# Kernel optimization log

Hardware: AMD Instinct MI355X
Metric: run time of the kernel (lower is better)

The kernel has to match this reference:

```python
import jax, jax.numpy as jnp
import numpy as np

R = 25          # regions (hard-coded [:25, 0] slice in the source)
NUM_CONSUMER = 27


def _ln(x, g, b, axes, eps):
    m = jnp.mean(x, axis=axes, keepdims=True)
    v = jnp.mean((x - m) ** 2, axis=axes, keepdims=True)
    return (x - m) / jnp.sqrt(v + eps) * g + b


def setup_inputs() -> dict:
    key = jax.random.key(0)
    n, c, h, e = 64, 64, 8, 1024
    bs = R
    ks = jax.random.split(key, 24)
    inp = {
        "business_structure_target": jax.random.normal(ks[0], (bs, c, n, 4), jnp.float32),
        "business_structure_infected": jax.random.normal(ks[1], (bs, c, n, 4), jnp.float32),
        "customer_structure_target": jax.random.uniform(ks[2], (bs, c, n, NUM_CONSUMER, 4), jnp.float32),
        "customer_structure_infected": jax.random.uniform(ks[3], (bs, c, n, NUM_CONSUMER, 4), jnp.float32),
        "index_target_idx": jax.random.randint(ks[4], (bs, c), 0, R, jnp.int32),
        "index_infected_idx": jax.random.randint(ks[5], (bs, c), 0, R, jnp.int32),
        "covid_outbreak_business": jax.random.randint(ks[6], (bs, c), 0, n, jnp.int32),
        # parameters
        "emb_weight": jax.random.normal(ks[7], (R * n, e), jnp.float32),
        "emb_ln_g": jnp.ones((e,), jnp.float32),
        "emb_ln_b": jnp.zeros((e,), jnp.float32),
        "WQ_t": jax.random.normal(ks[8], (h, e, e), jnp.float32) / np.sqrt(e),
        "WK_t": jax.random.normal(ks[9], (h, e, e), jnp.float32) / np.sqrt(e),
        "WQ_i": jax.random.normal(ks[10], (h, e, e), jnp.float32) / np.sqrt(e),
        "WK_i": jax.random.normal(ks[11], (h, e, e), jnp.float32) / np.sqrt(e),
        "W_os": jax.random.normal(ks[12], (e, e), jnp.float32) / np.sqrt(e),
        "b_os": jnp.zeros((e,), jnp.float32),
        "BS_g": jnp.ones((c, n), jnp.float32), "BS_b": jnp.zeros((c, n), jnp.float32),
        "CS_g": jnp.ones((c, n), jnp.float32), "CS_b": jnp.zeros((c, n), jnp.float32),
        "OS_g": jnp.ones((c, n), jnp.float32), "OS_b": jnp.zeros((c, n), jnp.float32),
    }
    return inp


def _mha(emb_blocks, WQ, WK, indices):
    # emb_blocks: (R, n, e); indices: (d,)
    d = indices.shape[0]
    n, e = emb_blocks.shape[1], emb_blocks.shape[2]
    ew = emb_blocks[indices].reshape(d * n, e)           # gather district blocks
    Q = jnp.einsum('te,hfe->htf', ew, WQ).reshape(-1, d, n, e)  # torch Linear: x @ W.T
    K = jnp.einsum('te,hfe->htf', ew, WK).reshape(-1, d, n, e)
    QK = jnp.einsum('hdie,hdje->hdij', Q, K) / jnp.sqrt(jnp.float32(e))
    # torch Softmax(dim=1) on (d, n, n) -> normalize over the first industry axis
    return jax.nn.softmax(QK, axis=2)                    # (h, d, n, n)


def reference(business_structure_target, business_structure_infected,
              customer_structure_target, customer_structure_infected,
              index_target_idx, index_infected_idx, covid_outbreak_business,
              emb_weight, emb_ln_g, emb_ln_b,
              WQ_t, WK_t, WQ_i, WK_i, W_os, b_os,
              BS_g, BS_b, CS_g, CS_b, OS_g, OS_b):
    n = business_structure_target.shape[2]
    e = emb_weight.shape[1]

    bt = jnp.mean(business_structure_target, -1)[:R, 0]      # (R, n)
    bi = jnp.mean(business_structure_infected, -1)[0]        # (c, n)
    ct = jnp.mean(customer_structure_target, -1)[:R, 0]      # (R, n, 27)
    ci = jnp.mean(customer_structure_infected, -1)[0]        # (c, n, 27)

    emb_norm = _ln(emb_weight, emb_ln_g, emb_ln_b, -1, 1e-16)
    emb_blocks = emb_norm.reshape(R, n, e)

    idx_t = index_target_idx[:R, 0].astype(jnp.int32)        # (R,)
    idx_i = index_infected_idx[0].astype(jnp.int32)          # (c,)

    attn_t = _mha(emb_blocks, WQ_t, WK_t, idx_t)             # (h, R, n, n)
    BR_trg = jnp.einsum('di,hdij->djh', bt, attn_t)          # (R, n, h)
    attn_i = _mha(emb_blocks, WQ_i, WK_i, idx_i)             # (h, c, n, n)
    BR_inf = jnp.einsum('di,hdij->djh', bi, attn_i)          # (c, n, h)

    # cosine similarity over the head dim, broadcast (R,1,n,h) x (1,c,n,h)
    eps = 1e-15
    a = BR_trg[:, None]
    b = BR_inf[None]
    dot = jnp.sum(a * b, -1)
    na = jnp.maximum(jnp.sqrt(jnp.sum(a * a, -1)), eps)
    nb = jnp.maximum(jnp.sqrt(jnp.sum(b * b, -1)), eps)
    BS = dot / (na * nb)                                     # (R, c, n)

    # JSD-style customer-structure similarity
    lt = jax.nn.log_softmax(ct, -1)[:, None]                 # (R, 1, n, 27)
    li = jax.nn.log_softmax(ci, -1)[None]                    # (1, c, n, 27)
    M = jax.nn.log_softmax((lt + li) / 2, -1)
    expM = jnp.exp(M)
    # KLDivLoss(log_target=True): exp(target) * (target - input)
    kl_t = jnp.mean(expM * (M - lt), -1)
    kl_i = jnp.mean(expM * (M - li), -1)
    CS = -((kl_t + kl_i) / 2)                                # (R, c, n)

    # outbreak-business similarity
    cov_buz = covid_outbreak_business[0].astype(jnp.int32)   # (c,)
    inf_emb_idx = idx_i * n + cov_buz
    ob_emb = emb_weight[inf_emb_idx] @ W_os.T + b_os         # (c, e)
    OS = (ob_emb @ emb_weight.T).reshape(-1, R, n)           # (c, R, n)
    OS = jnp.transpose(OS, (1, 0, 2))                        # (R, c, n)

    BS = _ln(BS, BS_g, BS_b, (-2, -1), 1e-5)
    CS = _ln(CS, CS_g, CS_b, (-2, -1), 1e-5)
    OS = _ln(OS, OS_g, OS_b, (-2, -1), 1e-5)
    return (BS, CS, OS)
```

## Files before the change

### kernel.cpp

```cpp
#include <hip/hip_runtime.h>
#include <math.h>

#define RR 25
#define HH 8
#define EE 1024
#define NCN 27

typedef short bf16x8 __attribute__((ext_vector_type(8)));
typedef float f32x4 __attribute__((ext_vector_type(4)));
typedef unsigned short us4 __attribute__((ext_vector_type(4)));
typedef unsigned short us8 __attribute__((ext_vector_type(8)));

__device__ __forceinline__ unsigned short f2bf(float x) {
    union { float f; unsigned int u; } v; v.f = x;
    const unsigned int u = v.u;
    return (unsigned short)((u + 0x7fffu + ((u >> 16) & 1u)) >> 16);
}
__device__ __forceinline__ float bf2f(unsigned short h) {
    union { unsigned int u; float f; } v; v.u = ((unsigned int)h) << 16;
    return v.f;
}

__device__ __forceinline__ float block_reduce_sum_256(float v, float* red) {
#pragma unroll
    for (int off = 32; off > 0; off >>= 1) v += __shfl_down(v, off, 64);
    const int lane = threadIdx.x & 63, wid = threadIdx.x >> 6;
    if (lane == 0) red[wid] = v;
    __syncthreads();
    if (threadIdx.x == 0) red[0] = red[0] + red[1] + red[2] + red[3];
    __syncthreads();
    const float r = red[0];
    __syncthreads();
    return r;
}

#define WTEN 16777216ull
#define WHEAD 2097152ull

__global__ __launch_bounds__(256) void k_ln_emb(
    const float* __restrict__ emb, const float* __restrict__ g,
    const float* __restrict__ b, float* __restrict__ out,
    unsigned short* __restrict__ Apl)
{
    __shared__ float red[4];
    const int t = blockIdx.x;
    const float* row = emb + (size_t)t * EE;
    float4 x = reinterpret_cast<const float4*>(row)[threadIdx.x];
    float s = x.x + x.y + x.z + x.w;
    s = block_reduce_sum_256(s, red);
    const float m = s * (1.0f / 1024.0f);
    const float d0 = x.x - m, d1 = x.y - m, d2 = x.z - m, d3 = x.w - m;
    float sq = d0*d0 + d1*d1 + d2*d2 + d3*d3;
    sq = block_reduce_sum_256(sq, red);
    const float rs = rsqrtf(sq * (1.0f / 1024.0f) + 1e-16f);
    const float4 gv = reinterpret_cast<const float4*>(g)[threadIdx.x];
    const float4 bv = reinterpret_cast<const float4*>(b)[threadIdx.x];
    float o[4];
    o[0] = d0 * rs * gv.x + bv.x;
    o[1] = d1 * rs * gv.y + bv.y;
    o[2] = d2 * rs * gv.z + bv.z;
    o[3] = d3 * rs * gv.w + bv.w;
    float4 of; of.x = o[0]; of.y = o[1]; of.z = o[2]; of.w = o[3];
    reinterpret_cast<float4*>(out + (size_t)t * EE)[threadIdx.x] = of;
    us4 hv, lv;
#pragma unroll
    for (int j = 0; j < 4; ++j) {
        const unsigned short h = f2bf(o[j]);
        hv[j] = h; lv[j] = f2bf(o[j] - bf2f(h));
    }
    const int k0 = threadIdx.x * 4;
    const int kt = k0 >> 5, kc = (k0 >> 3) & 3, j0 = k0 & 7;
    const int lane = (t & 15) + 16 * kc;
    const size_t base = ((size_t)(kt * 100 + (t >> 4)) * 2) * 512 + lane * 8 + j0;
    *reinterpret_cast<us4*>(Apl + base)       = hv;
    *reinterpret_cast<us4*>(Apl + base + 512) = lv;
}

__global__ __launch_bounds__(256) void k_splitw(
    const float* __restrict__ w0, const float* __restrict__ w1,
    const float* __restrict__ w2, const float* __restrict__ w3,
    unsigned short* __restrict__ wsp)
{
    const int t = blockIdx.y;
    const float* src = (t == 0) ? w0 : ((t == 1) ? w1 : ((t == 2) ? w2 : w3));
    unsigned short* dst = wsp + (size_t)t * WTEN;
    const size_t q = (size_t)blockIdx.x * 256 + threadIdx.x;
    const float4 x = reinterpret_cast<const float4*>(src)[q];
    const float xf[4] = {x.x, x.y, x.z, x.w};
    us4 hv, lv;
#pragma unroll
    for (int j = 0; j < 4; ++j) {
        const unsigned short h = f2bf(xf[j]);
        hv[j] = h; lv[j] = f2bf(xf[j] - bf2f(h));
    }
    const size_t e4 = q * 4;
    const int h = (int)(e4 >> 20);
    const int rem = (int)(e4 & 1048575);
    const int f = rem >> 10, e = rem & 1023;
    const int kt = e >> 5, kc = (e >> 3) & 3, j0 = e & 7;
    const int lane = (f & 15) + 16 * kc;
    const size_t base = (size_t)h * WHEAD + ((size_t)(kt * 64 + (f >> 4)) * 2) * 512 + lane * 8 + j0;
    *reinterpret_cast<us4*>(dst + base)       = hv;
    *reinterpret_cast<us4*>(dst + base + 512) = lv;
}

__global__ __launch_bounds__(256) void k_proj2(
    const unsigned short* __restrict__ Apl,
    const unsigned short* __restrict__ Wpl,
    float* __restrict__ Qb, float* __restrict__ Kb)
{
    __shared__ __align__(16) unsigned short As_l[8 * 512];
    __shared__ __align__(16) unsigned short Bs_l[32 * 512];
    const int fid = blockIdx.x;
    const int xcd = fid & 7;
    const int iw = fid >> 3;
    const int z = xcd + (iw / 100) * 8;
    const int mb = iw % 100;
    const int by = mb >> 2, bx = mb & 3;
    const int pk = z >> 3, h = z & 7;
    const unsigned short* Wb = Wpl + (size_t)pk * WTEN + (size_t)h * WHEAD;
    float* C = (pk ? Kb : Qb) + (size_t)h * 1600 * EE;
    const int tid = threadIdx.x;
    const int lane = tid & 63, wv = tid >> 6;
    const int by4 = by * 4, bx16 = bx * 16;
    f32x4 acc[4][4] = {};
    for (int kt = 0; kt < 32; ++kt) {
        const unsigned short* aslab = Apl + ((size_t)(kt * 100 + by4)) * 1024;
        const unsigned short* bslab = Wb  + ((size_t)(kt * 64  + bx16)) * 1024;
        us8 ra0 = *reinterpret_cast<const us8*>(aslab + (size_t)tid * 8);
        us8 ra1 = *reinterpret_cast<const us8*>(aslab + (size_t)(256 + tid) * 8);
        us8 rb[8];
#pragma unroll
        for (int c = 0; c < 8; ++c)
            rb[c] = *reinterpret_cast<const us8*>(bslab + (size_t)(c * 256 + tid) * 8);
        __syncthreads();
        *reinterpret_cast<us8*>(As_l + tid * 8) = ra0;
        *reinterpret_cast<us8*>(As_l + (256 + tid) * 8) = ra1;
#pragma unroll
        for (int c = 0; c < 8; ++c)
            *reinterpret_cast<us8*>(Bs_l + (c * 256 + tid) * 8) = rb[c];
        __syncthreads();
        bf16x8 ah[4], al[4], bh[4], bl[4];
#pragma unroll
        for (int m = 0; m < 4; ++m) {
            ah[m] = *reinterpret_cast<const bf16x8*>(As_l + (m * 2 + 0) * 512 + lane * 8);
            al[m] = *reinterpret_cast<const bf16x8*>(As_l + (m * 2 + 1) * 512 + lane * 8);
        }
#pragma unroll
        for (int n = 0; n < 4; ++n) {
            const int nt = wv * 4 + n;
            bh[n] = *reinterpret_cast<const bf16x8*>(Bs_l + (nt * 2 + 0) * 512 + lane * 8);
            bl[n] = *reinterpret_cast<const bf16x8*>(Bs_l + (nt * 2 + 1) * 512 + lane * 8);
        }
#pragma unroll
        for (int m = 0; m < 4; ++m)
#pragma unroll
            for (int n = 0; n < 4; ++n) {
                acc[m][n] = __builtin_amdgcn_mfma_f32_16x16x32_bf16(ah[m], bh[n], acc[m][n], 0, 0, 0);
                acc[m][n] = __builtin_amdgcn_mfma_f32_16x16x32_bf16(ah[m], bl[n], acc[m][n], 0, 0, 0);
                acc[m][n] = __builtin_amdgcn_mfma_f32_16x16x32_bf16(al[m], bh[n], acc[m][n], 0, 0, 0);
            }
    }
    const int rg = lane >> 4, fr = lane & 15;
#pragma unroll
    for (int m = 0; m < 4; ++m)
#pragma unroll
        for (int n = 0; n < 4; ++n)
#pragma unroll
            for (int q = 0; q < 4; ++q) {
                const int row = by * 64 + m * 16 + rg * 4 + q;
                const int col = bx * 256 + wv * 64 + n * 16 + fr;
                C[(size_t)row * EE + col] = acc[m][n][q];
            }
}

struct SplitTiles {
    unsigned short Ah[64][40], Al[64][40], Bh[64][40], Bl[64][40];
};

#define MFMA_COMPUTE(SM)                                                         \
    {                                                                            \
        bf16x8 ah_[2], al_[2], bh_[2], bl_[2];                                   \
        _Pragma("unroll")                                                        \
        for (int m = 0; m < 2; ++m) {                                            \
            const int r = wr * 32 + m * 16 + fr;                                 \
            ah_[m] = *reinterpret_cast<const bf16x8*>(&(SM).Ah[r][ch * 8]);      \
            al_[m] = *reinterpret_cast<const bf16x8*>(&(SM).Al[r][ch * 8]);      \
        }                                                                        \
        _Pragma("unroll")                                                        \
        for (int n = 0; n < 2; ++n) {                                            \
            const int r = wc * 32 + n * 16 + fr;                                 \
            bh_[n] = *reinterpret_cast<const bf16x8*>(&(SM).Bh[r][ch * 8]);      \
            bl_[n] = *reinterpret_cast<const bf16x8*>(&(SM).Bl[r][ch * 8]);      \
        }                                                                        \
        _Pragma("unroll")                                                        \
        for (int m = 0; m < 2; ++m)                                              \
            _Pragma("unroll")                                                    \
            for (int n = 0; n < 2; ++n) {                                        \
                acc[m][n] = __builtin_amdgcn_mfma_f32_16x16x32_bf16(ah_[m], bh_[n], acc[m][n], 0, 0, 0); \
                acc[m][n] = __builtin_amdgcn_mfma_f32_16x16x32_bf16(ah_[m], bl_[n], acc[m][n], 0, 0, 0); \
                acc[m][n] = __builtin_amdgcn_mfma_f32_16x16x32_bf16(al_[m], bh_[n], acc[m][n], 0, 0, 0); \
            }                                                                    \
    }

#define MFMA_STAGE_SPLIT_GEN(AROW, BROW, SM)                                     \
    {                                                                            \
        float4 ra[2], rb[2];                                                     \
        _Pragma("unroll")                                                        \
        for (int l = 0; l < 2; ++l) {                                            \
            const int id = l * 256 + tid;                                        \
            const int row = id >> 3, c4 = (id & 7) * 4;                          \
            ra[l] = *reinterpret_cast<const float4*>((AROW(row)) + k0 + c4);     \
            rb[l] = *reinterpret_cast<const float4*>((BROW(row)) + k0 + c4);     \
        }                                                                        \
        __syncthreads();                                                         \
        _Pragma("unroll")                                                        \
        for (int l = 0; l < 2; ++l) {                                            \
            const int id = l * 256 + tid;                                        \
            const int row = id >> 3, c4 = (id & 7) * 4;                          \
            const float xa[4] = {ra[l].x, ra[l].y, ra[l].z, ra[l].w};            \
            const float xb[4] = {rb[l].x, rb[l].y, rb[l].z, rb[l].w};            \
            us4 ahv, alv, bhv, blv;                                              \
            _Pragma("unroll")                                                    \
            for (int j = 0; j < 4; ++j) {                                        \
                const unsigned short ha = f2bf(xa[j]);                           \
                ahv[j] = ha; alv[j] = f2bf(xa[j] - bf2f(ha));                    \
                const unsigned short hb = f2bf(xb[j]);                           \
                bhv[j] = hb; blv[j] = f2bf(xb[j] - bf2f(hb));                    \
            }                                                                    \
            *reinterpret_cast<us4*>(&(SM).Ah[row][c4]) = ahv;                    \
            *reinterpret_cast<us4*>(&(SM).Al[row][c4]) = alv;                    \
            *reinterpret_cast<us4*>(&(SM).Bh[row][c4]) = bhv;                    \
            *reinterpret_cast<us4*>(&(SM).Bl[row][c4]) = blv;                    \
        }                                                                        \
        __syncthreads();                                                         \
    }

__global__ __launch_bounds__(256) void k_proj_mfma(
    const float* __restrict__ A,
    const float* __restrict__ WQ, const float* __restrict__ WK,
    float* __restrict__ Qb, float* __restrict__ Kb, int qkHeadStride)
{
    __shared__ __align__(16) SplitTiles sm;
    const int h = blockIdx.z >> 1;
    const int pk = blockIdx.z & 1;
    const float* W = (pk ? WK : WQ) + (size_t)h * EE * EE;
    float* C = (pk ? Kb : Qb) + (size_t)h * qkHeadStride;
    const int bx = blockIdx.x, by = blockIdx.y;
    const int tid = threadIdx.x;
    const int lane = tid & 63, w = tid >> 6;
    const int wr = w >> 1, wc = w & 1;
    const int fr = lane & 15, ch = lane >> 4;
    const float* Abase = A + (size_t)by * 64 * EE;
    const float* Bbase = W + (size_t)bx * 64 * EE;
#define AROWP(r) (Abase + (size_t)(r) * EE)
#define BROWP(r) (Bbase + (size_t)(r) * EE)
    f32x4 acc[2][2] = {};
    for (int k0 = 0; k0 < EE; k0 += 32) {
        MFMA_STAGE_SPLIT_GEN(AROWP, BROWP, sm)
        MFMA_COMPUTE(sm)
    }
#undef AROWP
#undef BROWP
    const int rg = lane >> 4;
#pragma unroll
    for (int m = 0; m < 2; ++m)
#pragma unroll
        for (int n = 0; n < 2; ++n)
#pragma unroll
            for (int q = 0; q < 4; ++q) {
                const int row = by * 64 + wr * 32 + m * 16 + rg * 4 + q;
                const int col = bx * 64 + wc * 32 + n * 16 + fr;
                C[(size_t)row * EE + col] = acc[m][n][q];
            }
}

__global__ __launch_bounds__(256) void k_qk_mfma(
    const float* __restrict__ Qall, const float* __restrict__ Kall,
    float* __restrict__ attn_all, int qkHeadStride, int attnHeadStride)
{
    __shared__ __align__(16) union { SplitTiles t; float Ss[64][65]; } u;
    __shared__ float redm[4][64];
    __shared__ float reds[4][64];
    const int r = blockIdx.x;
    const int h = blockIdx.y;
    const float* Q = Qall + (size_t)h * qkHeadStride;
    const float* K = Kall + (size_t)h * qkHeadStride;
    float* attn = attn_all + (size_t)h * attnHeadStride + (size_t)r * 4096;
    const int tid = threadIdx.x;
    const int lane = tid & 63, w = tid >> 6;
    const int wr = w >> 1, wc = w & 1;
    const int fr = lane & 15, ch = lane >> 4;
    const float* Abase = Q + (size_t)r * 64 * EE;
    const float* Bbase = K + (size_t)r * 64 * EE;
#define AROWP(rr) (Abase + (size_t)(rr) * EE)
#define BROWP(rr) (Bbase + (size_t)(rr) * EE)
    f32x4 acc[2][2] = {};
    for (int k0 = 0; k0 < EE; k0 += 32) {
        MFMA_STAGE_SPLIT_GEN(AROWP, BROWP, u.t)
        MFMA_COMPUTE(u.t)
    }
#undef AROWP
#undef BROWP
    __syncthreads();
    const int rg = lane >> 4;
#pragma unroll
    for (int m = 0; m < 2; ++m)
#pragma unroll
        for (int n = 0; n < 2; ++n)
#pragma unroll
            for (int q = 0; q < 4; ++q)
                u.Ss[wr * 32 + m * 16 + rg * 4 + q][wc * 32 + n * 16 + fr] =
                    acc[m][n][q] * (1.0f / 32.0f);
    __syncthreads();
    const int j = tid & 63, seg = tid >> 6;
    float mx = -1e30f;
#pragma unroll
    for (int i = 0; i < 16; ++i) mx = fmaxf(mx, u.Ss[seg * 16 + i][j]);
    redm[seg][j] = mx;
    __syncthreads();
    const float cm = fmaxf(fmaxf(redm[0][j], redm[1][j]), fmaxf(redm[2][j], redm[3][j]));
    float ssum = 0.f;
#pragma unroll
    for (int i = 0; i < 16; ++i) {
        const float e = __expf(u.Ss[seg * 16 + i][j] - cm);
        u.Ss[seg * 16 + i][j] = e;
        ssum += e;
    }
    reds[seg][j] = ssum;
    __syncthreads();
    const float inv = 1.0f / (reds[0][j] + reds[1][j] + reds[2][j] + reds[3][j]);
#pragma unroll
    for (int i = 0; i < 16; ++i)
        attn[(seg * 16 + i) * 64 + j] = u.Ss[seg * 16 + i][j] * inv;
}

__global__ __launch_bounds__(64) void k_br(
    const float* __restrict__ bst, const float* __restrict__ bsi,
    const int* __restrict__ iti, const int* __restrict__ iii,
    const float* __restrict__ attn_t, const float* __restrict__ attn_i,
    float* __restrict__ br_t, float* __restrict__ br_i)
{
    __shared__ float bw[64];
    const int dp = blockIdx.x;
    const int h = blockIdx.y;
    const int j = threadIdx.x;
    const float* attn;
    float* out;
    if (dp < RR) {
        const int d = dp;
        const int rb = iti[d * 64];
        const float* p = bst + ((size_t)(d * 64) * 64 + j) * 4;
        bw[j] = 0.25f * (p[0] + p[1] + p[2] + p[3]);
        attn = attn_t + ((size_t)h * RR + rb) * 4096;
        out = br_t + (size_t)d * 64 * 8;
    } else {
        const int d = dp - RR;
        const int rb = iii[d];
        const float* p = bsi + ((size_t)d * 64 + j) * 4;
        bw[j] = 0.25f * (p[0] + p[1] + p[2] + p[3]);
        attn = attn_i + ((size_t)h * RR + rb) * 4096;
        out = br_i + (size_t)d * 64 * 8;
    }
    __syncthreads();
    float acc = 0.f;
#pragma unroll 8
    for (int i = 0; i < 64; ++i) acc += bw[i] * attn[i * 64 + j];
    out[(size_t)j * 8 + h] = acc;
}

__global__ __launch_bounds__(256) void k_bs(
    const float* __restrict__ br_t, const float* __restrict__ br_i,
    float* __restrict__ raw)
{
    const int p = blockIdx.x;
#pragma unroll
    for (int it = 0; it < 16; ++it) {
        const int o = it * 256 + threadIdx.x;
        const int q = o >> 6, j = o & 63;
        const float* a = br_t + ((size_t)p * 64 + j) * 8;
        const float* b = br_i + ((size_t)q * 64 + j) * 8;
        float dot = 0.f, sa = 0.f, sb = 0.f;
#pragma unroll
        for (int h = 0; h < 8; ++h) {
            const float va = a[h], vb = b[h];
            dot += va * vb; sa += va * va; sb += vb * vb;
        }
        const float na = fmaxf(sqrtf(sa), 1e-15f);
        const float nb = fmaxf(sqrtf(sb), 1e-15f);
        raw[(size_t)p * 4096 + o] = dot / (na * nb);
    }
}

__global__ __launch_bounds__(256) void k_lsm(
    const float* __restrict__ cst, const float* __restrict__ csi,
    float* __restrict__ lt, float* __restrict__ li)
{
    const int row = blockIdx.x * 256 + threadIdx.x;
    if (row >= 1600 + 4096) return;
    const float* src;
    float* dst;
    if (row < 1600) {
        const int d = row >> 6, i = row & 63;
        src = cst + ((size_t)(d * 64) * 64 + i) * NCN * 4;
        dst = lt + (size_t)row * NCN;
    } else {
        const int u = row - 1600;
        const int q = u >> 6, i = u & 63;
        src = csi + ((size_t)q * 64 + i) * NCN * 4;
        dst = li + (size_t)u * NCN;
    }
    float x[NCN];
    float m = -1e30f;
#pragma unroll
    for (int k = 0; k < NCN; ++k) {
        x[k] = 0.25f * (src[k*4] + src[k*4+1] + src[k*4+2] + src[k*4+3]);
        m = fmaxf(m, x[k]);
    }
    float s = 0.f;
#pragma unroll
    for (int k = 0; k < NCN; ++k) s += __expf(x[k] - m);
    const float lse = m + __logf(s);
#pragma unroll
    for (int k = 0; k < NCN; ++k) dst[k] = x[k] - lse;
}

__global__ __launch_bounds__(256) void k_cs(
    const float* __restrict__ lt, const float* __restrict__ li, float* __restrict__ raw)
{
    const int p = blockIdx.x;
    for (int it = 0; it < 16; ++it) {
        const int o = it * 256 + threadIdx.x;
        const int q = o >> 6, i = o & 63;
        const float* a = lt + ((size_t)p * 64 + i) * NCN;
        const float* b = li + ((size_t)q * 64 + i) * NCN;
        float la[NCN], lb[NCN];
        float m = -1e30f;
#pragma unroll
        for (int k = 0; k < NCN; ++k) {
            la[k] = a[k]; lb[k] = b[k];
            m = fmaxf(m, 0.5f * (la[k] + lb[k]));
        }
        float z = 0.f;
#pragma unroll
        for (int k = 0; k < NCN; ++k) z += __expf(0.5f * (la[k] + lb[k]) - m);
        const float lse = m + __logf(z);
        float kt = 0.f, ki = 0.f;
#pragma unroll
        for (int k = 0; k < NCN; ++k) {
            const float M = 0.5f * (la[k] + lb[k]) - lse;
            const float eM = __expf(M);
            kt += eM * (M - la[k]);
            ki += eM * (M - lb[k]);
        }
        raw[(size_t)p * 4096 + o] = -(kt + ki) * (0.5f / 27.0f);
    }
}

__global__ __launch_bounds__(256) void k_obemb2(
    const float* __restrict__ emb, const float* __restrict__ Wos,
    const float* __restrict__ bos, const int* __restrict__ iii,
    const int* __restrict__ cob, float* __restrict__ ob)
{
    __shared__ __align__(16) SplitTiles sm;
    __shared__ int gidx[64];
    const int bx = blockIdx.x;
    const int tid = threadIdx.x;
    const int lane = tid & 63, w = tid >> 6;
    const int wr = w >> 1, wc = w & 1;
    const int fr = lane & 15, ch = lane >> 4;
    if (tid < 64) gidx[tid] = iii[tid] * 64 + cob[tid];
    __syncthreads();
    const float* Bbase = Wos + (size_t)bx * 64 * EE;
#define AROWP(r) (emb + (size_t)gidx[(r)] * EE)
#define BROWP(r) (Bbase + (size_t)(r) * EE)
    f32x4 acc[2][2] = {};
    for (int k0 = 0; k0 < EE; k0 += 32) {
        MFMA_STAGE_SPLIT_GEN(AROWP, BROWP, sm)
        MFMA_COMPUTE(sm)
    }
#undef AROWP
#undef BROWP
    const int rg = lane >> 4;
#pragma unroll
    for (int m = 0; m < 2; ++m)
#pragma unroll
        for (int n = 0; n < 2; ++n)
#pragma unroll
            for (int q = 0; q < 4; ++q) {
                const int row = wr * 32 + m * 16 + rg * 4 + q;
                const int col = bx * 64 + wc * 32 + n * 16 + fr;
                ob[(size_t)row * EE + col] = acc[m][n][q] + bos[col];
            }
}

__global__ __launch_bounds__(256) void k_os2(
    const float* __restrict__ ob, const float* __restrict__ emb, float* __restrict__ raw)
{
    __shared__ __align__(16) SplitTiles sm;
    const int p = blockIdx.x;
    const int tid = threadIdx.x;
    const int lane = tid & 63, w = tid >> 6;
    const int wr = w >> 1, wc = w & 1;
    const int fr = lane & 15, ch = lane >> 4;
    const float* Bbase = emb + (size_t)p * 64 * EE;
#define AROWP(r) (ob + (size_t)(r) * EE)
#define BROWP(r) (Bbase + (size_t)(r) * EE)
    f32x4 acc[2][2] = {};
    for (int k0 = 0; k0 < EE; k0 += 32) {
        MFMA_STAGE_SPLIT_GEN(AROWP, BROWP, sm)
        MFMA_COMPUTE(sm)
    }
#undef AROWP
#undef BROWP
    const int rg = lane >> 4;
#pragma unroll
    for (int m = 0; m < 2; ++m)
#pragma unroll
        for (int n = 0; n < 2; ++n)
#pragma unroll
            for (int q = 0; q < 4; ++q) {
                const int row = wr * 32 + m * 16 + rg * 4 + q;
                const int col = wc * 32 + n * 16 + fr;
                raw[(size_t)p * 4096 + row * 64 + col] = acc[m][n][q];
            }
}

__global__ __launch_bounds__(256) void k_final_ln(
    const float* __restrict__ raw,
    const float* __restrict__ BSg, const float* __restrict__ BSb,
    const float* __restrict__ CSg, const float* __restrict__ CSb,
    const float* __restrict__ OSg, const float* __restrict__ OSb,
    float* __restrict__ out)
{
    __shared__ float red[4];
    const int s = blockIdx.x, p = blockIdx.y;
    const float* g  = (s == 0) ? BSg : ((s == 1) ? CSg : OSg);
    const float* bb = (s == 0) ? BSb : ((s == 1) ? CSb : OSb);
    const float* x = raw + ((size_t)s * RR + p) * 4096;
    float v[16];
    float sum = 0.f;
#pragma unroll
    for (int it = 0; it < 16; ++it) { v[it] = x[it * 256 + threadIdx.x]; sum += v[it]; }
    sum = block_reduce_sum_256(sum, red);
    const float m = sum * (1.0f / 4096.0f);
    float sq = 0.f;
#pragma unroll
    for (int it = 0; it < 16; ++it) { const float d = v[it] - m; sq += d * d; }
    sq = block_reduce_sum_256(sq, red);
    const float rs = rsqrtf(sq * (1.0f / 4096.0f) + 1e-5f);
    float* o = out + ((size_t)s * RR + p) * 4096;
#pragma unroll
    for (int it = 0; it < 16; ++it) {
        const int oo = it * 256 + threadIdx.x;
        o[oo] = (v[it] - m) * rs * g[oo] + bb[oo];
    }
}

extern "C" void kernel_launch(void* const* d_in, const int* in_sizes, int n_in,
                              void* d_out, int out_size, void* d_ws, size_t ws_size,
                              hipStream_t stream)
{
    const float* bst = (const float*)d_in[0];
    const float* bsi = (const float*)d_in[1];
    const float* cst = (const float*)d_in[2];
    const float* csi = (const float*)d_in[3];
    const int*   iti = (const int*)d_in[4];
    const int*   iii = (const int*)d_in[5];
    const int*   cob = (const int*)d_in[6];
    const float* embw = (const float*)d_in[7];
    const float* eg  = (const float*)d_in[8];
    const float* ebb = (const float*)d_in[9];
    const float* WQt = (const float*)d_in[10];
    const float* WKt = (const float*)d_in[11];
    const float* WQi = (const float*)d_in[12];
    const float* WKi = (const float*)d_in[13];
    const float* Wos = (const float*)d_in[14];
    const float* bos = (const float*)d_in[15];
    const float* BSg = (const float*)d_in[16];
    const float* BSb = (const float*)d_in[17];
    const float* CSg = (const float*)d_in[18];
    const float* CSb = (const float*)d_in[19];
    const float* OSg = (const float*)d_in[20];
    const float* OSb = (const float*)d_in[21];

    const size_t tailF  = 819200ull*2 + 12800 + 32768 + 43200 + 110592 + 65536 + 307200;
    const size_t baseF  = 1638400ull + 1638400;
    const size_t wspF   = 33554432ull;
    const size_t qk8F   = 2ull * 8 * 1600 * EE;
    const size_t needBig = (baseF + wspF + qk8F + tailF) * 4;
    const size_t needMid = (baseF + qk8F + tailF) * 4;
    const int tier = (ws_size >= needBig) ? 2 : ((ws_size >= needMid) ? 1 : 0);

    float* ws = (float*)d_ws;
    size_t cur = 0;
    float* emb_n = ws + cur;                               cur += 1638400;
    unsigned short* Apl = (unsigned short*)(ws + cur);     cur += 1638400;
    unsigned short* wsp = nullptr;
    if (tier == 2) { wsp = (unsigned short*)(ws + cur);    cur += wspF; }
    const size_t qkSz = (tier >= 1) ? (size_t)8 * 1600 * EE : (size_t)1600 * EE;
    float* Qbuf   = ws + cur;        cur += qkSz;
    float* Kbuf   = ws + cur;        cur += qkSz;
    float* attn_t = ws + cur;        cur += 819200;
    float* attn_i = ws + cur;        cur += 819200;
    float* br_t   = ws + cur;        cur += 12800;
    float* br_i   = ws + cur;        cur += 32768;
    float* lt     = ws + cur;        cur += 43200;
    float* li     = ws + cur;        cur += 110592;
    float* ob     = ws + cur;        cur += 65536;
    float* raw    = ws + cur;        cur += 307200;

    k_ln_emb<<<1600, 256, 0, stream>>>(embw, eg, ebb, emb_n, Apl);
    if (tier == 2)
        k_splitw<<<dim3(8192, 4), 256, 0, stream>>>(WQt, WKt, WQi, WKi, wsp);

    for (int w = 0; w < 2; ++w) {
        const float* WQ = w ? WQi : WQt;
        const float* WK = w ? WKi : WKt;
        float* attn = w ? attn_i : attn_t;
        if (tier == 2) {
            k_proj2<<<1600, 256, 0, stream>>>(Apl, wsp + (size_t)(2*w) * WTEN, Qbuf, Kbuf);
            k_qk_mfma<<<dim3(25, 8), 256, 0, stream>>>(Qbuf, Kbuf, attn, 1600 * EE, RR * 4096);
        } else if (tier == 1) {
            k_proj_mfma<<<dim3(16, 25, 16), 256, 0, stream>>>(emb_n, WQ, WK, Qbuf, Kbuf, 1600 * EE);
            k_qk_mfma<<<dim3(25, 8), 256, 0, stream>>>(Qbuf, Kbuf, attn, 1600 * EE, RR * 4096);
        } else {
            for (int h = 0; h < HH; ++h) {
                k_proj_mfma<<<dim3(16, 25, 2), 256, 0, stream>>>(
                    emb_n, WQ + (size_t)h * EE * EE, WK + (size_t)h * EE * EE, Qbuf, Kbuf, 0);
                k_qk_mfma<<<dim3(25, 1), 256, 0, stream>>>(
                    Qbuf, Kbuf, attn + (size_t)h * RR * 4096, 0, 0);
            }
        }
    }

    k_br<<<dim3(RR + 64, 8), 64, 0, stream>>>(bst, bsi, iti, iii, attn_t, attn_i, br_t, br_i);
    k_bs<<<25, 256, 0, stream>>>(br_t, br_i, raw);
    k_lsm<<<23, 256, 0, stream>>>(cst, csi, lt, li);
    k_cs<<<25, 256, 0, stream>>>(lt, li, raw + 102400);
    k_obemb2<<<16, 256, 0, stream>>>(embw, Wos, bos, iii, cob, ob);
    k_os2<<<25, 256, 0, stream>>>(ob, embw, raw + 204800);
    k_final_ln<<<dim3(3, RR), 256, 0, stream>>>(raw, BSg, BSb, CSg, CSb, OSg, OSb, (float*)d_out);
}
```

Measured before the change: 862.0 us.

## Double-buffer A tiles and load B fragments directly from global in projection GEMM

Reworks the projection GEMM main loop. The A tile is double-buffered in LDS with register prefetch of the next k-slab. The B (weight) fragments are now loaded straight from global into registers, so the B LDS staging buffer and one barrier per iteration are gone. Block indexing is also reordered so that consecutive blocks share a column tile (by fastest), which changes L2 reuse of the weights. This aims to overlap global loads with MFMA work and cut LDS traffic and synchronisation, at the cost of more registers and redundant loads on the last iteration.

```diff
diff --git a/kernel.cpp b/kernel.cpp
--- a/kernel.cpp
+++ b/kernel.cpp
@@ -109,58 +109,77 @@
     const unsigned short* __restrict__ Wpl,
     float* __restrict__ Qb, float* __restrict__ Kb)
 {
-    __shared__ __align__(16) unsigned short As_l[8 * 512];
-    __shared__ __align__(16) unsigned short Bs_l[32 * 512];
+    __shared__ __align__(16) unsigned short As_l[2][8 * 512];
     const int fid = blockIdx.x;
     const int xcd = fid & 7;
     const int iw = fid >> 3;
-    const int z = xcd + (iw / 100) * 8;
+    const int zsel = iw / 100;
     const int mb = iw % 100;
-    const int by = mb >> 2, bx = mb & 3;
-    const int pk = z >> 3, h = z & 7;
+    const int bx = mb / 25;
+    const int by = mb % 25;
+    const int pk = zsel, h = xcd;
     const unsigned short* Wb = Wpl + (size_t)pk * WTEN + (size_t)h * WHEAD;
     float* C = (pk ? Kb : Qb) + (size_t)h * 1600 * EE;
     const int tid = threadIdx.x;
     const int lane = tid & 63, wv = tid >> 6;
     const int by4 = by * 4, bx16 = bx * 16;
+    const int l8 = lane * 8;
+
     f32x4 acc[4][4] = {};
-    for (int kt = 0; kt < 32; ++kt) {
-        const unsigned short* aslab = Apl + ((size_t)(kt * 100 + by4)) * 1024;
-        const unsigned short* bslab = Wb  + ((size_t)(kt * 64  + bx16)) * 1024;
-        us8 ra0 = *reinterpret_cast<const us8*>(aslab + (size_t)tid * 8);
-        us8 ra1 = *reinterpret_cast<const us8*>(aslab + (size_t)(256 + tid) * 8);
-        us8 rb[8];
-#pragma unroll
-        for (int c = 0; c < 8; ++c)
-            rb[c] = *reinterpret_cast<const us8*>(bslab + (size_t)(c * 256 + tid) * 8);
-        __syncthreads();
-        *reinterpret_cast<us8*>(As_l + tid * 8) = ra0;
-        *reinterpret_cast<us8*>(As_l + (256 + tid) * 8) = ra1;
-#pragma unroll
-        for (int c = 0; c < 8; ++c)
-            *reinterpret_cast<us8*>(Bs_l + (c * 256 + tid) * 8) = rb[c];
-        __syncthreads();
-        bf16x8 ah[4], al[4], bh[4], bl[4];
-#pragma unroll
-        for (int m = 0; m < 4; ++m) {
-            ah[m] = *reinterpret_cast<const bf16x8*>(As_l + (m * 2 + 0) * 512 + lane * 8);
-            al[m] = *reinterpret_cast<const bf16x8*>(As_l + (m * 2 + 1) * 512 + lane * 8);
-        }
+    us8 aR0[2], aR1[2];
+    bf16x8 bR0[8], bR1[8];
+
+    {
+        const unsigned short* aslab = Apl + ((size_t)by4) * 1024;
+        const unsigned short* bslab = Wb + ((size_t)bx16) * 1024;
+        aR0[0] = *reinterpret_cast<const us8*>(aslab + (size_t)tid * 8);
+        aR0[1] = *reinterpret_cast<const us8*>(aslab + (size_t)(256 + tid) * 8);
 #pragma unroll
         for (int n = 0; n < 4; ++n) {
             const int nt = wv * 4 + n;
-            bh[n] = *reinterpret_cast<const bf16x8*>(Bs_l + (nt * 2 + 0) * 512 + lane * 8);
-            bl[n] = *reinterpret_cast<const bf16x8*>(Bs_l + (nt * 2 + 1) * 512 + lane * 8);
+            bR0[2*n]   = *reinterpret_cast<const bf16x8*>(bslab + (size_t)((nt*2 + 0) * 512) + l8);
+            bR0[2*n+1] = *reinterpret_cast<const bf16x8*>(bslab + (size_t)((nt*2 + 1) * 512) + l8);
         }
-#pragma unroll
-        for (int m = 0; m < 4; ++m)
-#pragma unroll
-            for (int n = 0; n < 4; ++n) {
-                acc[m][n] = __builtin_amdgcn_mfma_f32_16x16x32_bf16(ah[m], bh[n], acc[m][n], 0, 0, 0);
-                acc[m][n] = __builtin_amdgcn_mfma_f32_16x16x32_bf16(ah[m], bl[n], acc[m][n], 0, 0, 0);
-                acc[m][n] = __builtin_amdgcn_mfma_f32_16x16x32_bf16(al[m], bh[n], acc[m][n], 0, 0, 0);
-            }
-    }
+    }
+
+#define PROJ_PHASE(AC, BC, AN, BN, P, KT)                                        \
+    {                                                                            \
+        *reinterpret_cast<us8*>(&As_l[P][tid * 8]) = AC[0];                      \
+        *reinterpret_cast<us8*>(&As_l[P][(256 + tid) * 8]) = AC[1];              \
+        __syncthreads();                                                         \
+        const int ktn = ((KT) < 31) ? (KT) + 1 : 31;                             \
+        const unsigned short* aslabn = Apl + ((size_t)(ktn * 100 + by4)) * 1024; \
+        const unsigned short* bslabn = Wb + ((size_t)(ktn * 64 + bx16)) * 1024;  \
+        AN[0] = *reinterpret_cast<const us8*>(aslabn + (size_t)tid * 8);         \
+        AN[1] = *reinterpret_cast<const us8*>(aslabn + (size_t)(256 + tid) * 8); \
+        _Pragma("unroll")                                                        \
+        for (int n = 0; n < 4; ++n) {                                            \
+            const int nt = wv * 4 + n;                                           \
+            BN[2*n]   = *reinterpret_cast<const bf16x8*>(bslabn + (size_t)((nt*2 + 0) * 512) + l8); \
+            BN[2*n+1] = *reinterpret_cast<const bf16x8*>(bslabn + (size_t)((nt*2 + 1) * 512) + l8); \
+        }                                                                        \
+        bf16x8 ah[4], al[4];                                                     \
+        _Pragma("unroll")                                                        \
+        for (int m = 0; m < 4; ++m) {                                            \
+            ah[m] = *reinterpret_cast<const bf16x8*>(&As_l[P][(m*2 + 0) * 512 + l8]); \
+            al[m] = *reinterpret_cast<const bf16x8*>(&As_l[P][(m*2 + 1) * 512 + l8]); \
+        }                                                                        \
+        _Pragma("unroll")                                                        \
+        for (int m = 0; m < 4; ++m)                                              \
+            _Pragma("unroll")                                                    \
+            for (int n = 0; n < 4; ++n) {                                        \
+                acc[m][n] = __builtin_amdgcn_mfma_f32_16x16x32_bf16(ah[m], BC[2*n],   acc[m][n], 0, 0, 0); \
+                acc[m][n] = __builtin_amdgcn_mfma_f32_16x16x32_bf16(ah[m], BC[2*n+1], acc[m][n], 0, 0, 0); \
+                acc[m][n] = __builtin_amdgcn_mfma_f32_16x16x32_bf16(al[m], BC[2*n],   acc[m][n], 0, 0, 0); \
+            }                                                                    \
+    }
+
+    for (int kt = 0; kt < 32; kt += 2) {
+        PROJ_PHASE(aR0, bR0, aR1, bR1, 0, kt)
+        PROJ_PHASE(aR1, bR1, aR0, bR0, 1, kt + 1)
+    }
+#undef PROJ_PHASE
+
     const int rg = lane >> 4, fr = lane & 15;
 #pragma unroll
     for (int m = 0; m < 4; ++m)
```

After: 784.1 us. 9.0% less time.
